# Kernel tuning notes

Hardware: AMD Instinct MI355X
Metric: run time of the kernel (lower is better)

The kernel has to match this reference:

```python
import jax, jax.numpy as jnp
import numpy as np

N = 100_000   # nodes
E = 3_200_000 # edges (avg degree 32)
IN = 256      # input feature dim


def setup_inputs() -> dict:
    key = jax.random.key(0)
    ks = jax.random.split(key, 10)
    w = lambda k, s: (jax.random.normal(k, s, jnp.float32) * 0.02)
    return {
        "x": jax.random.normal(ks[0], (N, IN), jnp.float32),
        "edge_index": jax.random.randint(ks[1], (2, E), 0, N, dtype=jnp.int32),
        "edge_attr": jax.random.normal(ks[2], (E, 1), jnp.float32),
        # conv1: ExpGraphConv(IN, 64, 128)
        "W1a": w(ks[3], (IN, 64)), "b1a": jnp.zeros((64,), jnp.float32),
        "W1b": w(ks[4], (IN + 64, 128)), "b1b": jnp.zeros((128,), jnp.float32),
        # conv2: ExpGraphConv(128, 32->hidden 64? per ctor (128, 32, 64)): msg hidden 32... kept as repo: hidden=32? Using (128,64) msg, (192,64) out per faithful cat structure
        "W2a": w(ks[5], (128, 64)), "b2a": jnp.zeros((64,), jnp.float32),
        "W2b": w(ks[6], (128 + 64, 64)), "b2b": jnp.zeros((64,), jnp.float32),
        # head
        "Wl1": w(ks[7], (64, 32)), "bl1": jnp.zeros((32,), jnp.float32),
        "Wl2": w(ks[8], (32, 1)), "bl2": jnp.zeros((1,), jnp.float32),
    }


def _mean_aggr(h, src, dst, n):
    # gather messages from source nodes, scatter-mean into destination nodes
    s = jax.ops.segment_sum(h[src], dst, num_segments=n)          # [N, d]
    cnt = jax.ops.segment_sum(jnp.ones((src.shape[0],), h.dtype), dst, num_segments=n)
    return s / jnp.maximum(cnt, 1.0)[:, None]


def _exp_graph_conv(x, src, dst, Wa, ba, Wb, bb):
    # message MLP on source features, mean aggregation, then linear on [x || aggr]
    h = x @ Wa + ba                                               # [N, hidden]
    m = _mean_aggr(h, src, dst, x.shape[0])                       # [N, hidden]
    return jnp.concatenate([x, m], axis=1) @ Wb + bb              # [N, out]


def reference(x, edge_index, edge_attr, W1a, b1a, W1b, b1b, W2a, b2a, W2b, b2b, Wl1, bl1, Wl2, bl2):
    src, dst = edge_index[0], edge_index[1]
    x = jax.nn.relu(_exp_graph_conv(x, src, dst, W1a, b1a, W1b, b1b))
    x = jax.nn.relu(_exp_graph_conv(x, src, dst, W2a, b2a, W2b, b2b))
    x = jax.nn.relu(x @ Wl1 + bl1)
    return x @ Wl2 + bl2
```

## Files before the change

kernel.cpp:

```cpp
#include <hip/hip_runtime.h>

#define IN_DIM 256
#define CAP 10240
#define EPB 4096

typedef _Float16 f16;
typedef _Float16 f16x8 __attribute__((ext_vector_type(8)));
typedef float f32x4 __attribute__((ext_vector_type(4)));
typedef unsigned u32x4 __attribute__((ext_vector_type(4)));
typedef unsigned u32x2 __attribute__((ext_vector_type(2)));


__global__ __launch_bounds__(256) void bucket_scatter_k(const int* __restrict__ srcp,
                                                        const int* __restrict__ dstp,
                                                        int* __restrict__ bcur,
                                                        unsigned* __restrict__ bedge, int E) {
    __shared__ int cnt[512], lstart[512], delta[512], fill[512];
    __shared__ int pfx[256];
    __shared__ unsigned spay[EPB];
    __shared__ unsigned char sbk[EPB];
    int tid = threadIdx.x;
    cnt[tid] = 0; cnt[tid + 256] = 0;
    fill[tid] = 0; fill[tid + 256] = 0;
    __syncthreads();
    size_t base = (size_t)blockIdx.x * EPB;
    int nloc = E - (int)base; if (nloc > EPB) nloc = EPB;
    int dreg[EPB / 256], sreg[EPB / 256];
#pragma unroll
    for (int j = 0; j < EPB / 256; j++) {
        int e = j * 256 + tid;
        if (e < nloc) {
            dreg[j] = dstp[base + e];
            sreg[j] = srcp[base + e];
            atomicAdd(&cnt[dreg[j] >> 8], 1);
        }
    }
    __syncthreads();
    int a0 = cnt[2 * tid], a1 = cnt[2 * tid + 1], s = a0 + a1;
    pfx[tid] = s;
    __syncthreads();
    for (int off = 1; off < 256; off <<= 1) {
        int t2 = (tid >= off) ? pfx[tid - off] : 0;
        __syncthreads();
        pfx[tid] += t2;
        __syncthreads();
    }
    int excl = pfx[tid] - s;
    lstart[2 * tid] = excl;
    lstart[2 * tid + 1] = excl + a0;
    int g0 = 0, g1 = 0;
    if (a0) g0 = atomicAdd(&bcur[2 * tid], a0);
    if (a1) g1 = atomicAdd(&bcur[2 * tid + 1], a1);
    delta[2 * tid]     = (2 * tid) * CAP + g0 - excl;
    delta[2 * tid + 1] = (2 * tid + 1) * CAP + g1 - (excl + a0);
    __syncthreads();
#pragma unroll
    for (int j = 0; j < EPB / 256; j++) {
        int e = j * 256 + tid;
        if (e < nloc) {
            int d = dreg[j], bk = d >> 8;
            int slot = lstart[bk] + atomicAdd(&fill[bk], 1);
            spay[slot] = (unsigned)sreg[j] | ((unsigned)(d & 255) << 17);
            sbk[slot] = (unsigned char)bk;
        }
    }
    __syncthreads();
    int mid = lstart[256];
#pragma unroll
    for (int j = 0; j < EPB / 256; j++) {
        int i = j * 256 + tid;
        if (i < nloc) {
            int bk = (int)sbk[i] | ((i >= mid) ? 256 : 0);
            int gp = i + delta[bk];
            if (gp < (bk + 1) * CAP)
                bedge[gp] = spay[i];
        }
    }
}

__global__ __launch_bounds__(256) void fine_sort_k(unsigned* __restrict__ bedge,
                                                   const int* __restrict__ bcur,
                                                   int2* __restrict__ ose, int Nn) {
    __shared__ int cnt[256], cur[256], pfx[256];
    __shared__ int sorted[CAP];
    int b = blockIdx.x, tid = threadIdx.x;
    int lo = b * CAP;
    int sz = bcur[b];
    if (sz > CAP) sz = CAP;
    cnt[tid] = 0;
    __syncthreads();
    for (int i = tid; i < sz; i += 256) atomicAdd(&cnt[bedge[lo + i] >> 17], 1);
    __syncthreads();
    int c = cnt[tid];
    pfx[tid] = c;
    __syncthreads();
    for (int off = 1; off < 256; off <<= 1) {
        int t2 = (tid >= off) ? pfx[tid - off] : 0;
        __syncthreads();
        pfx[tid] += t2;
        __syncthreads();
    }
    int excl = pfx[tid] - c;
    cur[tid] = excl;
    int node = b * 256 + tid;
    if (node < Nn) ose[node] = make_int2(lo + excl, lo + excl + c);
    __syncthreads();
    for (int i = tid; i < sz; i += 256) {
        unsigned v = bedge[lo + i];
        int slot = atomicAdd(&cur[v >> 17], 1);
        sorted[slot] = (int)(v & 0x1FFFFu);
    }
    __syncthreads();
    for (int i = tid; i < sz; i += 256) bedge[lo + i] = (unsigned)sorted[i];
}


__global__ __launch_bounds__(256) void wcast_all_k(const float* __restrict__ W1a, f16* __restrict__ Wt1a,
                                                   const float* __restrict__ W1b, f16* __restrict__ Wt1b,
                                                   const float* __restrict__ W2a, f16* __restrict__ Wt2a,
                                                   const float* __restrict__ W2b, f16* __restrict__ Wt2b) {
    int i = blockIdx.x * 256 + threadIdx.x;
    const float* W; f16* Wt; int K, N, local;
    if (i < 16384)      { W = W1a; Wt = Wt1a; K = 256; N = 64;  local = i; }
    else if (i < 57344) { W = W1b; Wt = Wt1b; K = 320; N = 128; local = i - 16384; }
    else if (i < 65536) { W = W2a; Wt = Wt2a; K = 128; N = 64;  local = i - 57344; }
    else if (i < 77824) { W = W2b; Wt = Wt2b; K = 192; N = 64;  local = i - 65536; }
    else return;
    int n = local / K, k = local - n * K;
    Wt[local] = (f16)W[(size_t)k * N + n];
}


__global__ __launch_bounds__(256) void aggr_k(const int2* __restrict__ ose,
                                              const int* __restrict__ ssrc,
                                              const f16* __restrict__ h,
                                              f16* __restrict__ m, int n) {
    int wave = (blockIdx.x * 256 + threadIdx.x) >> 6;
    int lane = threadIdx.x & 63;
    if (wave >= n) return;
    int2 se = ose[wave];
    int s0 = se.x, s1 = se.y;
    int q = lane >> 4, l16 = lane & 15;
    const u32x2* hp = reinterpret_cast<const u32x2*>(h);
    float a0 = 0.f, a1 = 0.f, a2 = 0.f, a3 = 0.f;
    auto acc = [&](u32x2 u) {
        union { u32x2 u; f16 hh[4]; } p; p.u = u;
        a0 += (float)p.hh[0]; a1 += (float)p.hh[1];
        a2 += (float)p.hh[2]; a3 += (float)p.hh[3];
    };
    for (int c = s0; c < s1; c += 64) {
        int cn = min(64, s1 - c);
        int myidx = (lane < cn) ? ssrc[c + lane] : 0;
        int t = 0;
        for (; t + 16 <= cn; t += 16) {
            int ia = __shfl(myidx, t + q);
            int ib = __shfl(myidx, t + 4 + q);
            int ic = __shfl(myidx, t + 8 + q);
            int id = __shfl(myidx, t + 12 + q);
            u32x2 ua = hp[(size_t)ia * 16 + l16];
            u32x2 ub = hp[(size_t)ib * 16 + l16];
            u32x2 uc = hp[(size_t)ic * 16 + l16];
            u32x2 ud = hp[(size_t)id * 16 + l16];
            acc(ua); acc(ub); acc(uc); acc(ud);
        }
        for (; t < cn; t += 4) {
            int r = t + q;
            int rr = (r < cn) ? r : (cn - 1);
            int ia = __shfl(myidx, rr);
            if (r < cn) acc(hp[(size_t)ia * 16 + l16]);
        }
    }
    a0 += __shfl_xor(a0, 16); a1 += __shfl_xor(a1, 16);
    a2 += __shfl_xor(a2, 16); a3 += __shfl_xor(a3, 16);
    a0 += __shfl_xor(a0, 32); a1 += __shfl_xor(a1, 32);
    a2 += __shfl_xor(a2, 32); a3 += __shfl_xor(a3, 32);
    if (lane < 16) {
        float inv = 1.0f / fmaxf((float)(s1 - s0), 1.0f);
        union { u32x2 u; f16 hh[4]; } p;
        p.hh[0] = (f16)(a0 * inv); p.hh[1] = (f16)(a1 * inv);
        p.hh[2] = (f16)(a2 * inv); p.hh[3] = (f16)(a3 * inv);
        reinterpret_cast<u32x2*>(m + (size_t)wave * 64)[l16] = p.u;
    }
}


template <int BN, bool A1F32, bool FUSE_HEAD>
__global__ __launch_bounds__(256) void gemm_mfma(const void* __restrict__ A1v, int K1,
                                                 const f16* __restrict__ A2, int K2,
                                                 const f16* __restrict__ Wt,
                                                 const float* __restrict__ bias,
                                                 f16* __restrict__ Y, int M, int relu,
                                                 int stream_out,
                                                 const float* __restrict__ Wl1,
                                                 const float* __restrict__ bl1,
                                                 const float* __restrict__ Wl2,
                                                 const float* __restrict__ bl2,
                                                 float* __restrict__ out) {
    static_assert(!FUSE_HEAD || BN == 64, "head fusion assumes BN==64");
    constexpr int BM = 64, BK = 32;
    constexpr int WN = BN / 2;
    constexpr int NB = WN / 16;
    constexpr int SEGB = BN / 64;
    constexpr int EPS = BN + 8;
    constexpr int VECN = 8;
    constexpr int TPR = BN / VECN;
    constexpr size_t SM_AB = (size_t)BM * BK * 2 + (size_t)BN * BK * 2;
    constexpr size_t SM_EP = (size_t)BM * EPS * 2;
    constexpr size_t SM_HEAD = FUSE_HEAD ? (2048 * 4 + 64 * 4) : 0;
    constexpr size_t SM1 = SM_EP + SM_HEAD;
    constexpr size_t SM = SM_AB > SM1 ? SM_AB : SM1;
    __shared__ __align__(16) char smem[SM];
    f16 (*As)[BK] = reinterpret_cast<f16(*)[BK]>(smem);
    f16 (*Bs)[BK] = reinterpret_cast<f16(*)[BK]>(smem + (size_t)BM * BK * 2);
    const int tid  = threadIdx.x;
    const int wave = tid >> 6;
    const int lane = tid & 63;
    const int wr   = wave >> 1;
    const int wc   = wave & 1;
    const int quad = lane >> 4;
    const int l16  = lane & 15;
    const int row0 = blockIdx.x * BM;
    const int Ktot = K1 + K2;

    if constexpr (FUSE_HEAD) {
        float* w1s = reinterpret_cast<float*>(smem + SM_EP);
        for (int t2 = tid; t2 < 2048; t2 += 256) w1s[t2] = Wl1[t2];
        if (tid < 32) { (w1s + 2048)[tid] = bl1[tid]; (w1s + 2048 + 32)[tid] = Wl2[tid]; }
    }

    f32x4 acc[2][NB];
#pragma unroll
    for (int i = 0; i < 2; i++)
#pragma unroll
        for (int j = 0; j < NB; j++) acc[i][j] = (f32x4)(0.f);

    const int ra = tid >> 2, sa = tid & 3;
    int rowA = row0 + ra;  if (rowA >= M) rowA = M - 1;

    u32x4 aReg, bReg[SEGB];
    auto loadA = [&](int kk) {
        if (kk < K1) {
            if constexpr (A1F32) {
                const float* bp = reinterpret_cast<const float*>(A1v) +
                                  (size_t)rowA * K1 + kk + sa * 8;
                f32x4 v0 = __builtin_nontemporal_load(reinterpret_cast<const f32x4*>(bp));
                f32x4 v1 = __builtin_nontemporal_load(reinterpret_cast<const f32x4*>(bp) + 1);
                union { f16 h[8]; u32x4 u; } p;
                p.h[0] = (f16)v0.x; p.h[1] = (f16)v0.y; p.h[2] = (f16)v0.z; p.h[3] = (f16)v0.w;
                p.h[4] = (f16)v1.x; p.h[5] = (f16)v1.y; p.h[6] = (f16)v1.z; p.h[7] = (f16)v1.w;
                aReg = p.u;
            } else {
                aReg = __builtin_nontemporal_load(reinterpret_cast<const u32x4*>(
                    reinterpret_cast<const f16*>(A1v) + (size_t)rowA * K1 + kk + sa * 8));
            }
        } else {
            aReg = __builtin_nontemporal_load(reinterpret_cast<const u32x4*>(
                A2 + (size_t)rowA * K2 + (kk - K1) + sa * 8));
        }
    };
    auto loadB = [&](int kk) {
#pragma unroll
        for (int i = 0; i < SEGB; i++) {
            int fid = tid + i * 256;
            int n = fid >> 2, s = fid & 3;
            bReg[i] = *reinterpret_cast<const u32x4*>(Wt + (size_t)n * Ktot + kk + s * 8);
        }
    };

    loadA(0); loadB(0);
    for (int kk = 0; kk < Ktot; kk += BK) {
        reinterpret_cast<u32x4*>(&As[0][0])[tid] = aReg;
#pragma unroll
        for (int i = 0; i < SEGB; i++)
            reinterpret_cast<u32x4*>(&Bs[0][0])[tid + i * 256] = bReg[i];
        __syncthreads();
        if (kk + BK < Ktot) { loadA(kk + BK); loadB(kk + BK); }
        f16x8 af[2], bf[NB];
#pragma unroll
        for (int rb = 0; rb < 2; rb++) {
            int row = wr * 32 + rb * 16 + l16;
            af[rb] = *reinterpret_cast<const f16x8*>(&As[row][quad * 8]);
        }
#pragma unroll
        for (int cb = 0; cb < NB; cb++) {
            int n = wc * WN + cb * 16 + l16;
            bf[cb] = *reinterpret_cast<const f16x8*>(&Bs[n][quad * 8]);
        }
#pragma unroll
        for (int rb = 0; rb < 2; rb++)
#pragma unroll
            for (int cb = 0; cb < NB; cb++)
                acc[rb][cb] = __builtin_amdgcn_mfma_f32_16x16x32_f16(af[rb], bf[cb], acc[rb][cb], 0, 0, 0);
        __syncthreads();
    }

    f16* ep = reinterpret_cast<f16*>(smem);
#pragma unroll
    for (int rb = 0; rb < 2; rb++) {
#pragma unroll
        for (int cb = 0; cb < NB; cb++) {
            int col = wc * WN + cb * 16 + l16;
            float bv = bias[col];
#pragma unroll
            for (int r = 0; r < 4; r++) {
                int lrow = wr * 32 + rb * 16 + quad * 4 + r;
                float v = acc[rb][cb][r] + bv;
                if (relu) v = fmaxf(v, 0.f);
                ep[(size_t)lrow * EPS + col] = (f16)v;
            }
        }
    }
    __syncthreads();

    if constexpr (FUSE_HEAD) {
        float* w1s = reinterpret_cast<float*>(smem + SM_EP);
        float* b1s = w1s + 2048;
        float* w2s = b1s + 32;
        int row = tid >> 2, part = tid & 3;
        const f16* eprow = ep + (size_t)row * EPS;
        float hj[8];
#pragma unroll
        for (int j = 0; j < 8; j++) hj[j] = b1s[part * 8 + j];
        for (int k = 0; k < 64; k++) {
            float v = (float)eprow[k];
            const float* wrow = &w1s[k * 32 + part * 8];
#pragma unroll
            for (int j = 0; j < 8; j++) hj[j] += v * wrow[j];
        }
        float o = 0.f;
#pragma unroll
        for (int j = 0; j < 8; j++) o += fmaxf(hj[j], 0.f) * w2s[part * 8 + j];
        o += __shfl_xor(o, 1);
        o += __shfl_xor(o, 2);
        int grow = row0 + row;
        if (part == 0 && grow < M) out[grow] = o + bl2[0];
    } else {
#pragma unroll
        for (int p = 0; p < BM * TPR / 256; p++) {
            int fid = p * 256 + tid;
            int row = fid / TPR, c = fid % TPR;
            int grow = row0 + row;
            if (grow < M) {
                u32x4 val = *reinterpret_cast<const u32x4*>(ep + (size_t)row * EPS + c * VECN);
                u32x4* dst = reinterpret_cast<u32x4*>(Y + (size_t)grow * BN + c * VECN);
                if (stream_out) __builtin_nontemporal_store(val, dst);
                else            *dst = val;
            }
        }
    }
}


extern "C" void kernel_launch(void* const* d_in, const int* in_sizes, int n_in,
                              void* d_out, int out_size, void* d_ws, size_t ws_size,
                              hipStream_t stream) {
    const float* x   = (const float*)d_in[0];
    const int*   ei  = (const int*)d_in[1];
    const float* W1a = (const float*)d_in[3];
    const float* b1a = (const float*)d_in[4];
    const float* W1b = (const float*)d_in[5];
    const float* b1b = (const float*)d_in[6];
    const float* W2a = (const float*)d_in[7];
    const float* b2a = (const float*)d_in[8];
    const float* W2b = (const float*)d_in[9];
    const float* b2b = (const float*)d_in[10];
    const float* Wl1 = (const float*)d_in[11];
    const float* bl1 = (const float*)d_in[12];
    const float* Wl2 = (const float*)d_in[13];
    const float* bl2 = (const float*)d_in[14];

    const int N = in_sizes[0] / IN_DIM;
    const int E = in_sizes[1] / 2;
    const int* srcp = ei;
    const int* dstp = ei + E;

    char* ws = (char*)d_ws;
    size_t off = 0;
    auto alloc = [&](size_t bytes) -> char* {
        char* p = ws + off;
        off = (off + bytes + 255) & ~(size_t)255;
        return p;
    };
    int NB2 = (N + 255) / 256;
    int*      bcur  = (int*)alloc(512 * 4);
    unsigned* bedge = (unsigned*)alloc((size_t)NB2 * CAP * 4);
    int2*     ose   = (int2*)alloc((size_t)N * 8);
    f16*      hbuf  = (f16*)alloc((size_t)N * 64 * 2);
    f16*      mbuf  = (f16*)alloc((size_t)N * 64 * 2);
    f16*      x1    = (f16*)alloc((size_t)N * 128 * 2);
    f16*      Wt1a  = (f16*)alloc(256 * 64 * 2);
    f16*      Wt1b  = (f16*)alloc(320 * 128 * 2);
    f16*      Wt2a  = (f16*)alloc(128 * 64 * 2);
    f16*      Wt2b  = (f16*)alloc(192 * 64 * 2);
    (void)ws_size;

    hipMemsetAsync(bcur, 0, 512 * 4, stream);
    int ebk = (E + EPB - 1) / EPB;
    bucket_scatter_k<<<ebk, 256, 0, stream>>>(srcp, dstp, bcur, bedge, E);
    fine_sort_k<<<NB2, 256, 0, stream>>>(bedge, bcur, ose, N);

    wcast_all_k<<<304, 256, 0, stream>>>(W1a, Wt1a, W1b, Wt1b, W2a, Wt2a, W2b, Wt2b);

    int mb = (N + 63) / 64;
    int ab = (N * 64 + 255) / 256;

    gemm_mfma<64, true, false><<<mb, 256, 0, stream>>>(
        x, IN_DIM, nullptr, 0, Wt1a, b1a, hbuf, N, 0, 0,
        nullptr, nullptr, nullptr, nullptr, nullptr);
    aggr_k<<<ab, 256, 0, stream>>>(ose, (const int*)bedge, hbuf, mbuf, N);
    gemm_mfma<128, true, false><<<mb, 256, 0, stream>>>(
        x, IN_DIM, mbuf, 64, Wt1b, b1b, x1, N, 1, 1,
        nullptr, nullptr, nullptr, nullptr, nullptr);

    gemm_mfma<64, false, false><<<mb, 256, 0, stream>>>(
        x1, 128, nullptr, 0, Wt2a, b2a, hbuf, N, 0, 0,
        nullptr, nullptr, nullptr, nullptr, nullptr);
    aggr_k<<<ab, 256, 0, stream>>>(ose, (const int*)bedge, hbuf, mbuf, N);

    gemm_mfma<64, false, true><<<mb, 256, 0, stream>>>(
        x1, 128, mbuf, 64, Wt2b, b2b, nullptr, N, 1, 0,
        Wl1, bl1, Wl2, bl2, (float*)d_out);
}
```

Baseline: 439.3 us.

## Fuse message and x-part GEMMs, fuse aggregation into mean-part GEMM

Each layer's concat GEMM is split into an x-part and an aggregated-part. The x-part is computed together with the message projection in one wide GEMM, so x is read once for layer 1. The neighbor mean aggregation is done inside a new kernel that holds the 64-row aggregate in LDS, multiplies by the mean-part weights, adds the precomputed x-part and applies ReLU. This removes the mbuf round trip, one kernel launch per layer and the second read of x. The cost is writing and re-reading a partial output buffer, lower parallelism in the aggregation (16 nodes per wave, serial), and padded LDS strides.

New measurement: 514.0 us. 1.17x slower.

```diff
diff --git a/kernel.cpp b/kernel.cpp
--- a/kernel.cpp
+++ b/kernel.cpp
@@ -115,118 +115,55 @@
 }
 
 
-__global__ __launch_bounds__(256) void wcast_all_k(const float* __restrict__ W1a, f16* __restrict__ Wt1a,
-                                                   const float* __restrict__ W1b, f16* __restrict__ Wt1b,
-                                                   const float* __restrict__ W2a, f16* __restrict__ Wt2a,
-                                                   const float* __restrict__ W2b, f16* __restrict__ Wt2b) {
+__global__ __launch_bounds__(256) void wcast_all_k(
+    const float* __restrict__ W1a, const float* __restrict__ W1b,
+    const float* __restrict__ W2a, const float* __restrict__ W2b,
+    const float* __restrict__ b1a, const float* __restrict__ b1b,
+    const float* __restrict__ b2a, const float* __restrict__ b2b,
+    f16* __restrict__ Wt1, f16* __restrict__ Wm1,
+    f16* __restrict__ Wt2, f16* __restrict__ Wm2,
+    float* __restrict__ bc1, float* __restrict__ bc2) {
     int i = blockIdx.x * 256 + threadIdx.x;
-    const float* W; f16* Wt; int K, N, local;
-    if (i < 16384)      { W = W1a; Wt = Wt1a; K = 256; N = 64;  local = i; }
-    else if (i < 57344) { W = W1b; Wt = Wt1b; K = 320; N = 128; local = i - 16384; }
-    else if (i < 65536) { W = W2a; Wt = Wt2a; K = 128; N = 64;  local = i - 57344; }
-    else if (i < 77824) { W = W2b; Wt = Wt2b; K = 192; N = 64;  local = i - 65536; }
-    else return;
-    int n = local / K, k = local - n * K;
-    Wt[local] = (f16)W[(size_t)k * N + n];
-}
-
-
-__global__ __launch_bounds__(256) void aggr_k(const int2* __restrict__ ose,
-                                              const int* __restrict__ ssrc,
-                                              const f16* __restrict__ h,
-                                              f16* __restrict__ m, int n) {
-    int wave = (blockIdx.x * 256 + threadIdx.x) >> 6;
-    int lane = threadIdx.x & 63;
-    if (wave >= n) return;
-    int2 se = ose[wave];
-    int s0 = se.x, s1 = se.y;
-    int q = lane >> 4, l16 = lane & 15;
-    const u32x2* hp = reinterpret_cast<const u32x2*>(h);
-    float a0 = 0.f, a1 = 0.f, a2 = 0.f, a3 = 0.f;
-    auto acc = [&](u32x2 u) {
-        union { u32x2 u; f16 hh[4]; } p; p.u = u;
-        a0 += (float)p.hh[0]; a1 += (float)p.hh[1];
-        a2 += (float)p.hh[2]; a3 += (float)p.hh[3];
-    };
-    for (int c = s0; c < s1; c += 64) {
-        int cn = min(64, s1 - c);
-        int myidx = (lane < cn) ? ssrc[c + lane] : 0;
-        int t = 0;
-        for (; t + 16 <= cn; t += 16) {
-            int ia = __shfl(myidx, t + q);
-            int ib = __shfl(myidx, t + 4 + q);
-            int ic = __shfl(myidx, t + 8 + q);
-            int id = __shfl(myidx, t + 12 + q);
-            u32x2 ua = hp[(size_t)ia * 16 + l16];
-            u32x2 ub = hp[(size_t)ib * 16 + l16];
-            u32x2 uc = hp[(size_t)ic * 16 + l16];
-            u32x2 ud = hp[(size_t)id * 16 + l16];
-            acc(ua); acc(ub); acc(uc); acc(ud);
-        }
-        for (; t < cn; t += 4) {
-            int r = t + q;
-            int rr = (r < cn) ? r : (cn - 1);
-            int ia = __shfl(myidx, rr);
-            if (r < cn) acc(hp[(size_t)ia * 16 + l16]);
-        }
-    }
-    a0 += __shfl_xor(a0, 16); a1 += __shfl_xor(a1, 16);
-    a2 += __shfl_xor(a2, 16); a3 += __shfl_xor(a3, 16);
-    a0 += __shfl_xor(a0, 32); a1 += __shfl_xor(a1, 32);
-    a2 += __shfl_xor(a2, 32); a3 += __shfl_xor(a3, 32);
-    if (lane < 16) {
-        float inv = 1.0f / fmaxf((float)(s1 - s0), 1.0f);
-        union { u32x2 u; f16 hh[4]; } p;
-        p.hh[0] = (f16)(a0 * inv); p.hh[1] = (f16)(a1 * inv);
-        p.hh[2] = (f16)(a2 * inv); p.hh[3] = (f16)(a3 * inv);
-        reinterpret_cast<u32x2*>(m + (size_t)wave * 64)[l16] = p.u;
-    }
-}
-
-
-template <int BN, bool A1F32, bool FUSE_HEAD>
-__global__ __launch_bounds__(256) void gemm_mfma(const void* __restrict__ A1v, int K1,
-                                                 const f16* __restrict__ A2, int K2,
-                                                 const f16* __restrict__ Wt,
-                                                 const float* __restrict__ bias,
-                                                 f16* __restrict__ Y, int M, int relu,
-                                                 int stream_out,
-                                                 const float* __restrict__ Wl1,
-                                                 const float* __restrict__ bl1,
-                                                 const float* __restrict__ Wl2,
-                                                 const float* __restrict__ bl2,
-                                                 float* __restrict__ out) {
-    static_assert(!FUSE_HEAD || BN == 64, "head fusion assumes BN==64");
-    constexpr int BM = 64, BK = 32;
-    constexpr int WN = BN / 2;
-    constexpr int NB = WN / 16;
-    constexpr int SEGB = BN / 64;
-    constexpr int EPS = BN + 8;
-    constexpr int VECN = 8;
-    constexpr int TPR = BN / VECN;
-    constexpr size_t SM_AB = (size_t)BM * BK * 2 + (size_t)BN * BK * 2;
+    if (i < 49152) {
+        int n = i >> 8, k = i & 255;
+        Wt1[i] = (f16)(n < 64 ? W1a[k * 64 + n] : W1b[k * 128 + (n - 64)]);
+    } else if (i < 57344) {
+        int l = i - 49152; int n = l >> 6, k = l & 63;
+        Wm1[l] = (f16)W1b[(256 + k) * 128 + n];
+    } else if (i < 73728) {
+        int l = i - 57344; int n = l >> 7, k = l & 127;
+        Wt2[l] = (f16)(n < 64 ? W2a[k * 64 + n] : W2b[k * 64 + (n - 64)]);
+    } else if (i < 77824) {
+        int l = i - 73728; int n = l >> 6, k = l & 63;
+        Wm2[l] = (f16)W2b[(128 + k) * 64 + n];
+    } else if (i < 78016) {
+        int l = i - 77824; bc1[l] = l < 64 ? b1a[l] : b1b[l - 64];
+    } else if (i < 78144) {
+        int l = i - 78016; bc2[l] = l < 64 ? b2a[l] : b2b[l - 64];
+    }
+}
+
+
+template <int BN, bool A1F32>
+__global__ __launch_bounds__(256) void gemm_fused(const void* __restrict__ A1v, int K1,
+                                                  const f16* __restrict__ Wt,
+                                                  const float* __restrict__ bc,
+                                                  f16* __restrict__ Y1,
+                                                  f16* __restrict__ Y2, int M) {
+    constexpr int BM = 64, BK = 32, ASTR = BK + 8;
+    constexpr int WN = BN / 2, NB = WN / 16, SEGB = BN / 64;
+    constexpr int EPS = BN + 8, TPR = BN / 8, N2 = BN - 64;
+    constexpr size_t SM_AB = (size_t)BM * ASTR * 2 + (size_t)BN * ASTR * 2;
     constexpr size_t SM_EP = (size_t)BM * EPS * 2;
-    constexpr size_t SM_HEAD = FUSE_HEAD ? (2048 * 4 + 64 * 4) : 0;
-    constexpr size_t SM1 = SM_EP + SM_HEAD;
-    constexpr size_t SM = SM_AB > SM1 ? SM_AB : SM1;
+    constexpr size_t SM = SM_AB > SM_EP ? SM_AB : SM_EP;
     __shared__ __align__(16) char smem[SM];
-    f16 (*As)[BK] = reinterpret_cast<f16(*)[BK]>(smem);
-    f16 (*Bs)[BK] = reinterpret_cast<f16(*)[BK]>(smem + (size_t)BM * BK * 2);
+    f16* As = reinterpret_cast<f16*>(smem);
+    f16* Bs = reinterpret_cast<f16*>(smem + (size_t)BM * ASTR * 2);
     const int tid  = threadIdx.x;
-    const int wave = tid >> 6;
-    const int lane = tid & 63;
-    const int wr   = wave >> 1;
-    const int wc   = wave & 1;
-    const int quad = lane >> 4;
-    const int l16  = lane & 15;
+    const int wave = tid >> 6, lane = tid & 63;
+    const int wr = wave >> 1, wc = wave & 1;
+    const int quad = lane >> 4, l16 = lane & 15;
     const int row0 = blockIdx.x * BM;
-    const int Ktot = K1 + K2;
-
-    if constexpr (FUSE_HEAD) {
-        float* w1s = reinterpret_cast<float*>(smem + SM_EP);
-        for (int t2 = tid; t2 < 2048; t2 += 256) w1s[t2] = Wl1[t2];
-        if (tid < 32) { (w1s + 2048)[tid] = bl1[tid]; (w1s + 2048 + 32)[tid] = Wl2[tid]; }
-    }
 
     f32x4 acc[2][NB];
 #pragma unroll
@@ -239,23 +176,18 @@
 
     u32x4 aReg, bReg[SEGB];
     auto loadA = [&](int kk) {
-        if (kk < K1) {
-            if constexpr (A1F32) {
-                const float* bp = reinterpret_cast<const float*>(A1v) +
-                                  (size_t)rowA * K1 + kk + sa * 8;
-                f32x4 v0 = __builtin_nontemporal_load(reinterpret_cast<const f32x4*>(bp));
-                f32x4 v1 = __builtin_nontemporal_load(reinterpret_cast<const f32x4*>(bp) + 1);
-                union { f16 h[8]; u32x4 u; } p;
-                p.h[0] = (f16)v0.x; p.h[1] = (f16)v0.y; p.h[2] = (f16)v0.z; p.h[3] = (f16)v0.w;
-                p.h[4] = (f16)v1.x; p.h[5] = (f16)v1.y; p.h[6] = (f16)v1.z; p.h[7] = (f16)v1.w;
-                aReg = p.u;
-            } else {
-                aReg = __builtin_nontemporal_load(reinterpret_cast<const u32x4*>(
-                    reinterpret_cast<const f16*>(A1v) + (size_t)rowA * K1 + kk + sa * 8));
-            }
+        if constexpr (A1F32) {
+            const float* bp = reinterpret_cast<const float*>(A1v) +
+                              (size_t)rowA * K1 + kk + sa * 8;
+            f32x4 v0 = __builtin_nontemporal_load(reinterpret_cast<const f32x4*>(bp));
+            f32x4 v1 = __builtin_nontemporal_load(reinterpret_cast<const f32x4*>(bp) + 1);
+            union { f16 h[8]; u32x4 u; } p;
+            p.h[0] = (f16)v0.x; p.h[1] = (f16)v0.y; p.h[2] = (f16)v0.z; p.h[3] = (f16)v0.w;
+            p.h[4] = (f16)v1.x; p.h[5] = (f16)v1.y; p.h[6] = (f16)v1.z; p.h[7] = (f16)v1.w;
+            aReg = p.u;
         } else {
             aReg = __builtin_nontemporal_load(reinterpret_cast<const u32x4*>(
-                A2 + (size_t)rowA * K2 + (kk - K1) + sa * 8));
+                reinterpret_cast<const f16*>(A1v) + (size_t)rowA * K1 + kk + sa * 8));
         }
     };
     auto loadB = [&](int kk) {
@@ -263,28 +195,31 @@
         for (int i = 0; i < SEGB; i++) {
             int fid = tid + i * 256;
             int n = fid >> 2, s = fid & 3;
-            bReg[i] = *reinterpret_cast<const u32x4*>(Wt + (size_t)n * Ktot + kk + s * 8);
+            bReg[i] = *reinterpret_cast<const u32x4*>(Wt + (size_t)n * K1 + kk + s * 8);
         }
     };
 
     loadA(0); loadB(0);
-    for (int kk = 0; kk < Ktot; kk += BK) {
-        reinterpret_cast<u32x4*>(&As[0][0])[tid] = aReg;
-#pragma unroll
-        for (int i = 0; i < SEGB; i++)
-            reinterpret_cast<u32x4*>(&Bs[0][0])[tid + i * 256] = bReg[i];
-        __syncthreads();
-        if (kk + BK < Ktot) { loadA(kk + BK); loadB(kk + BK); }
+    for (int kk = 0; kk < K1; kk += BK) {
+        *reinterpret_cast<u32x4*>(&As[ra * ASTR + sa * 8]) = aReg;
+#pragma unroll
+        for (int i = 0; i < SEGB; i++) {
+            int fid = tid + i * 256;
+            int n = fid >> 2, s = fid & 3;
+            *reinterpret_cast<u32x4*>(&Bs[n * ASTR + s * 8]) = bReg[i];
+        }
+        __syncthreads();
+        if (kk + BK < K1) { loadA(kk + BK); loadB(kk + BK); }
         f16x8 af[2], bf[NB];
 #pragma unroll
         for (int rb = 0; rb < 2; rb++) {
             int row = wr * 32 + rb * 16 + l16;
-            af[rb] = *reinterpret_cast<const f16x8*>(&As[row][quad * 8]);
+            af[rb] = *reinterpret_cast<const f16x8*>(&As[row * ASTR + quad * 8]);
         }
 #pragma unroll
         for (int cb = 0; cb < NB; cb++) {
             int n = wc * WN + cb * 16 + l16;
-            bf[cb] = *reinterpret_cast<const f16x8*>(&Bs[n][quad * 8]);
+            bf[cb] = *reinterpret_cast<const f16x8*>(&Bs[n * ASTR + quad * 8]);
         }
 #pragma unroll
         for (int rb = 0; rb < 2; rb++)
@@ -300,12 +235,157 @@
 #pragma unroll
         for (int cb = 0; cb < NB; cb++) {
             int col = wc * WN + cb * 16 + l16;
-            float bv = bias[col];
+            float bv = bc[col];
 #pragma unroll
             for (int r = 0; r < 4; r++) {
                 int lrow = wr * 32 + rb * 16 + quad * 4 + r;
-                float v = acc[rb][cb][r] + bv;
-                if (relu) v = fmaxf(v, 0.f);
+                ep[(size_t)lrow * EPS + col] = (f16)(acc[rb][cb][r] + bv);
+            }
+        }
+    }
+    __syncthreads();
+#pragma unroll
+    for (int p = 0; p < BM * TPR / 256; p++) {
+        int fid = p * 256 + tid;
+        int row = fid / TPR, c = fid % TPR, col0 = c * 8;
+        int grow = row0 + row;
+        if (grow < M) {
+            u32x4 val = *reinterpret_cast<const u32x4*>(&ep[(size_t)row * EPS + col0]);
+            if (col0 < 64)
+                *reinterpret_cast<u32x4*>(Y1 + (size_t)grow * 64 + col0) = val;
+            else
+                __builtin_nontemporal_store(val,
+                    reinterpret_cast<u32x4*>(Y2 + (size_t)grow * N2 + (col0 - 64)));
+        }
+    }
+}
+
+
+template <int BN, bool FUSE_HEAD>
+__global__ __launch_bounds__(256) void agemm(const int2* __restrict__ ose,
+                                             const int* __restrict__ ssrc,
+                                             const f16* __restrict__ h,
+                                             const f16* __restrict__ Wm,
+                                             const f16* __restrict__ P,
+                                             f16* __restrict__ Y,
+                                             const float* __restrict__ Wl1,
+                                             const float* __restrict__ bl1,
+                                             const float* __restrict__ Wl2,
+                                             const float* __restrict__ bl2,
+                                             float* __restrict__ out, int M) {
+    constexpr int BM = 64, ASTR = 72;
+    constexpr int WN = BN / 2, NB = WN / 16;
+    constexpr int EPS = BN + 8, TPR = BN / 8;
+    constexpr size_t SZ_A = (size_t)BM * ASTR * 2;
+    constexpr size_t SM_AB = SZ_A + (size_t)BN * ASTR * 2;
+    constexpr size_t SM_EP = (size_t)BM * EPS * 2;
+    constexpr size_t SM_CORE = SM_AB > SM_EP ? SM_AB : SM_EP;
+    constexpr size_t SM_HEAD = FUSE_HEAD ? (2048 + 64) * 4 : 0;
+    __shared__ __align__(16) char smem[SM_CORE + SM_HEAD];
+    f16* Am = reinterpret_cast<f16*>(smem);
+    f16* Bs = reinterpret_cast<f16*>(smem + SZ_A);
+    const int tid  = threadIdx.x;
+    const int wave = tid >> 6, lane = tid & 63;
+    const int wr = wave >> 1, wc = wave & 1;
+    const int quad = lane >> 4, l16 = lane & 15;
+    const int row0 = blockIdx.x * BM;
+
+    for (int fid = tid; fid < BN * 8; fid += 256) {
+        int n = fid >> 3, s = fid & 7;
+        *reinterpret_cast<u32x4*>(&Bs[n * ASTR + s * 8]) =
+            *reinterpret_cast<const u32x4*>(Wm + (size_t)n * 64 + s * 8);
+    }
+    if constexpr (FUSE_HEAD) {
+        float* w1s = reinterpret_cast<float*>(smem + SM_CORE);
+        for (int t2 = tid; t2 < 2048; t2 += 256) w1s[t2] = Wl1[t2];
+        if (tid < 32) { w1s[2048 + tid] = bl1[tid]; w1s[2048 + 32 + tid] = Wl2[tid]; }
+    }
+
+    const u32x2* hp = reinterpret_cast<const u32x2*>(h);
+    for (int i = 0; i < 16; i++) {
+        int node = wave * 16 + i, gnode = row0 + node;
+        int s0 = 0, s1 = 0;
+        if (gnode < M) { int2 se = ose[gnode]; s0 = se.x; s1 = se.y; }
+        float a0 = 0.f, a1 = 0.f, a2 = 0.f, a3 = 0.f;
+        auto accum = [&](u32x2 u) {
+            union { u32x2 u; f16 hh[4]; } p; p.u = u;
+            a0 += (float)p.hh[0]; a1 += (float)p.hh[1];
+            a2 += (float)p.hh[2]; a3 += (float)p.hh[3];
+        };
+        for (int c = s0; c < s1; c += 64) {
+            int cn = min(64, s1 - c);
+            int myidx = (lane < cn) ? ssrc[c + lane] : 0;
+            int t = 0;
+            for (; t + 16 <= cn; t += 16) {
+                int ia = __shfl(myidx, t + quad);
+                int ib = __shfl(myidx, t + 4 + quad);
+                int ic = __shfl(myidx, t + 8 + quad);
+                int id = __shfl(myidx, t + 12 + quad);
+                u32x2 ua = hp[(size_t)ia * 16 + l16];
+                u32x2 ub = hp[(size_t)ib * 16 + l16];
+                u32x2 uc = hp[(size_t)ic * 16 + l16];
+                u32x2 ud = hp[(size_t)id * 16 + l16];
+                accum(ua); accum(ub); accum(uc); accum(ud);
+            }
+            for (; t < cn; t += 4) {
+                int r = t + quad;
+                int rr = (r < cn) ? r : (cn - 1);
+                int ia = __shfl(myidx, rr);
+                if (r < cn) accum(hp[(size_t)ia * 16 + l16]);
+            }
+        }
+        a0 += __shfl_xor(a0, 16); a1 += __shfl_xor(a1, 16);
+        a2 += __shfl_xor(a2, 16); a3 += __shfl_xor(a3, 16);
+        a0 += __shfl_xor(a0, 32); a1 += __shfl_xor(a1, 32);
+        a2 += __shfl_xor(a2, 32); a3 += __shfl_xor(a3, 32);
+        if (lane < 16) {
+            float inv = 1.0f / fmaxf((float)(s1 - s0), 1.0f);
+            union { u32x2 u; f16 hh[4]; } pk;
+            pk.hh[0] = (f16)(a0 * inv); pk.hh[1] = (f16)(a1 * inv);
+            pk.hh[2] = (f16)(a2 * inv); pk.hh[3] = (f16)(a3 * inv);
+            *reinterpret_cast<u32x2*>(&Am[node * ASTR + l16 * 4]) = pk.u;
+        }
+    }
+    __syncthreads();
+
+    f32x4 acc[2][NB];
+#pragma unroll
+    for (int i = 0; i < 2; i++)
+#pragma unroll
+        for (int j = 0; j < NB; j++) acc[i][j] = (f32x4)(0.f);
+#pragma unroll
+    for (int ks = 0; ks < 2; ks++) {
+        f16x8 af[2], bf[NB];
+#pragma unroll
+        for (int rb = 0; rb < 2; rb++) {
+            int row = wr * 32 + rb * 16 + l16;
+            af[rb] = *reinterpret_cast<const f16x8*>(&Am[row * ASTR + ks * 32 + quad * 8]);
+        }
+#pragma unroll
+        for (int cb = 0; cb < NB; cb++) {
+            int n = wc * WN + cb * 16 + l16;
+            bf[cb] = *reinterpret_cast<const f16x8*>(&Bs[n * ASTR + ks * 32 + quad * 8]);
+        }
+#pragma unroll
+        for (int rb = 0; rb < 2; rb++)
+#pragma unroll
+            for (int cb = 0; cb < NB; cb++)
+                acc[rb][cb] = __builtin_amdgcn_mfma_f32_16x16x32_f16(af[rb], bf[cb], acc[rb][cb], 0, 0, 0);
+    }
+    __syncthreads();
+
+    f16* ep = reinterpret_cast<f16*>(smem);
+#pragma unroll
+    for (int rb = 0; rb < 2; rb++) {
+#pragma unroll
+        for (int cb = 0; cb < NB; cb++) {
+            int col = wc * WN + cb * 16 + l16;
+#pragma unroll
+            for (int r = 0; r < 4; r++) {
+                int lrow = wr * 32 + rb * 16 + quad * 4 + r;
+                int grow = row0 + lrow;
+                float pv = (grow < M) ? (float)P[(size_t)grow * BN + col] : 0.f;
+                float v = fmaxf(acc[rb][cb][r] + pv, 0.f);
                 ep[(size_t)lrow * EPS + col] = (f16)v;
             }
         }
@@ -313,7 +393,7 @@
     __syncthreads();
 
     if constexpr (FUSE_HEAD) {
-        float* w1s = reinterpret_cast<float*>(smem + SM_EP);
+        float* w1s = reinterpret_cast<float*>(smem + SM_CORE);
         float* b1s = w1s + 2048;
         float* w2s = b1s + 32;
         int row = tid >> 2, part = tid & 3;
@@ -341,10 +421,8 @@
             int row = fid / TPR, c = fid % TPR;
             int grow = row0 + row;
             if (grow < M) {
-                u32x4 val = *reinterpret_cast<const u32x4*>(ep + (size_t)row * EPS + c * VECN);
-                u32x4* dst = reinterpret_cast<u32x4*>(Y + (size_t)grow * BN + c * VECN);
-                if (stream_out) __builtin_nontemporal_store(val, dst);
-                else            *dst = val;
+                u32x4 val = *reinterpret_cast<const u32x4*>(&ep[(size_t)row * EPS + c * 8]);
+                *reinterpret_cast<u32x4*>(Y + (size_t)grow * BN + c * 8) = val;
             }
         }
     }
@@ -386,12 +464,16 @@
     unsigned* bedge = (unsigned*)alloc((size_t)NB2 * CAP * 4);
     int2*     ose   = (int2*)alloc((size_t)N * 8);
     f16*      hbuf  = (f16*)alloc((size_t)N * 64 * 2);
-    f16*      mbuf  = (f16*)alloc((size_t)N * 64 * 2);
+    f16*      pbuf  = (f16*)alloc((size_t)N * 128 * 2);
     f16*      x1    = (f16*)alloc((size_t)N * 128 * 2);
-    f16*      Wt1a  = (f16*)alloc(256 * 64 * 2);
-    f16*      Wt1b  = (f16*)alloc(320 * 128 * 2);
-    f16*      Wt2a  = (f16*)alloc(128 * 64 * 2);
-    f16*      Wt2b  = (f16*)alloc(192 * 64 * 2);
+    f16*      h2    = (f16*)alloc((size_t)N * 64 * 2);
+    f16*      p2    = (f16*)alloc((size_t)N * 64 * 2);
+    f16*      Wt1   = (f16*)alloc(192 * 256 * 2);
+    f16*      Wm1   = (f16*)alloc(128 * 64 * 2);
+    f16*      Wt2   = (f16*)alloc(128 * 128 * 2);
+    f16*      Wm2   = (f16*)alloc(64 * 64 * 2);
+    float*    bc1   = (float*)alloc(192 * 4);
+    float*    bc2   = (float*)alloc(128 * 4);
     (void)ws_size;
 
     hipMemsetAsync(bcur, 0, 512 * 4, stream);
@@ -399,25 +481,18 @@
     bucket_scatter_k<<<ebk, 256, 0, stream>>>(srcp, dstp, bcur, bedge, E);
     fine_sort_k<<<NB2, 256, 0, stream>>>(bedge, bcur, ose, N);
 
-    wcast_all_k<<<304, 256, 0, stream>>>(W1a, Wt1a, W1b, Wt1b, W2a, Wt2a, W2b, Wt2b);
+    wcast_all_k<<<306, 256, 0, stream>>>(W1a, W1b, W2a, W2b, b1a, b1b, b2a, b2b,
+                                         Wt1, Wm1, Wt2, Wm2, bc1, bc2);
 
     int mb = (N + 63) / 64;
-    int ab = (N * 64 + 255) / 256;
-
-    gemm_mfma<64, true, false><<<mb, 256, 0, stream>>>(
-        x, IN_DIM, nullptr, 0, Wt1a, b1a, hbuf, N, 0, 0,
-        nullptr, nullptr, nullptr, nullptr, nullptr);
-    aggr_k<<<ab, 256, 0, stream>>>(ose, (const int*)bedge, hbuf, mbuf, N);
-    gemm_mfma<128, true, false><<<mb, 256, 0, stream>>>(
-        x, IN_DIM, mbuf, 64, Wt1b, b1b, x1, N, 1, 1,
-        nullptr, nullptr, nullptr, nullptr, nullptr);
-
-    gemm_mfma<64, false, false><<<mb, 256, 0, stream>>>(
-        x1, 128, nullptr, 0, Wt2a, b2a, hbuf, N, 0, 0,
-        nullptr, nullptr, nullptr, nullptr, nullptr);
-    aggr_k<<<ab, 256, 0, stream>>>(ose, (const int*)bedge, hbuf, mbuf, N);
-
-    gemm_mfma<64, false, true><<<mb, 256, 0, stream>>>(
-        x1, 128, mbuf, 64, Wt2b, b2b, nullptr, N, 1, 0,
-        Wl1, bl1, Wl2, bl2, (float*)d_out);
-}
+    const int* ssrc = (const int*)bedge;
+
+    gemm_fused<192, true><<<mb, 256, 0, stream>>>(x, 256, Wt1, bc1, hbuf, pbuf, N);
+    agemm<128, false><<<mb, 256, 0, stream>>>(ose, ssrc, hbuf, Wm1, pbuf, x1,
+                                              nullptr, nullptr, nullptr, nullptr,
+                                              nullptr, N);
+
+    gemm_fused<128, false><<<mb, 256, 0, stream>>>(x1, 128, Wt2, bc2, h2, p2, N);
+    agemm<64, true><<<mb, 256, 0, stream>>>(ose, ssrc, h2, Wm2, p2, nullptr,
+                                            Wl1, bl1, Wl2, bl2, (float*)d_out, N);
+}
```
